# Kernel tuning notes

Measured on AMD Instinct MI355X. Metric: run time of the kernel, lower is better.

## Reference

```python
import jax, jax.numpy as jnp
import numpy as np
from jax import lax

N = 100000
E = 1600000
IN_C = 128
HID = 128
OUT_C = 64
NUM_CLASSES = 40
BN_EPS = 1e-5


def gcn_conv(x, row, col, W, b):
    # x: [N, F_in] -> [N, F_out]; PyG GCNConv: self-loops + sym normalization
    h = x @ W                                   # [N, F_out]
    loops = jnp.arange(N, dtype=row.dtype)
    r = jnp.concatenate([row, loops])           # [E+N]
    c = jnp.concatenate([col, loops])
    ones = jnp.ones(r.shape[0], dtype=x.dtype)
    deg = jax.ops.segment_sum(ones, c, num_segments=N)
    dinv = jnp.where(deg > 0, lax.rsqrt(deg), jnp.zeros_like(deg))
    norm = dinv[r] * dinv[c]                    # [E+N]
    msg = h[r] * norm[:, None]                  # gather + scale  [E+N, F_out]
    out = jax.ops.segment_sum(msg, c, num_segments=N)
    return out + b


def setup_inputs() -> dict:
    key = jax.random.key(0)
    ks = jax.random.split(key, 16)
    def glorot(k, shape):
        lim = float(np.sqrt(6.0 / (shape[0] + shape[1])))
        return jax.random.uniform(k, shape, jnp.float32, -lim, lim)
    x = jax.random.normal(ks[0], (N, IN_C), jnp.float32)
    edge_index = jax.random.randint(ks[1], (2, E), 0, N, jnp.int64)
    return {
        "x": x,
        "edge_index": edge_index,
        "w1": glorot(ks[2], (IN_C, HID)), "b1": jnp.zeros((HID,), jnp.float32),
        "w2": glorot(ks[3], (HID, HID)), "b2": jnp.zeros((HID,), jnp.float32),
        "bn_gamma": jnp.ones((HID,), jnp.float32), "bn_beta": jnp.zeros((HID,), jnp.float32),
        "bn_mean": jnp.zeros((HID,), jnp.float32), "bn_var": jnp.ones((HID,), jnp.float32),
        "cls_w": glorot(ks[4], (HID, OUT_C)), "cls_b": jnp.zeros((OUT_C,), jnp.float32),
        "sim_w": glorot(ks[5], (HID, NUM_CLASSES)), "sim_b": jnp.zeros((NUM_CLASSES,), jnp.float32),
        "hom_w": glorot(ks[6], (HID, 1)), "hom_b": jnp.zeros((1,), jnp.float32),
        "ent_w": glorot(ks[7], (HID, 1)), "ent_b": jnp.zeros((1,), jnp.float32),
    }


def reference(x, edge_index, w1, b1, w2, b2, bn_gamma, bn_beta, bn_mean, bn_var,
              cls_w, cls_b, sim_w, sim_b, hom_w, hom_b, ent_w, ent_b):
    row, col = edge_index[0], edge_index[1]
    # layer 1: GCNConv -> BN (eval) -> ReLU (dropout is identity in eval)
    h = gcn_conv(x, row, col, w1, b1)
    h = (h - bn_mean) * lax.rsqrt(bn_var + BN_EPS) * bn_gamma + bn_beta
    h = jax.nn.relu(h)
    # layer 2
    h = gcn_conv(h, row, col, w2, b2)
    main_out = jax.nn.log_softmax(h @ cls_w + cls_b, axis=1)
    sim_out = jax.nn.softmax(h @ sim_w + sim_b, axis=1)
    hom_out = jax.nn.sigmoid((h @ hom_w + hom_b)[:, 0])
    ent_out = jax.nn.sigmoid((h @ ent_w + ent_b)[:, 0])
    return (main_out, sim_out, hom_out, ent_out)
```

## Files before the change

kernel.cpp:

```cpp
#include <hip/hip_runtime.h>
#include <hip/hip_bf16.h>
#include <math.h>

#define N_NODES 100000
#define N_EDGES 1600000
#define F 128
#define OUT_C 64
#define NUM_CLASSES 40
#define BN_EPS 1e-5f

#define NBUCK 782
#define BCAP 4096

#define PREP_FILL 512
#define EPB ((N_EDGES + PREP_FILL - 1) / PREP_FILL)
#define FILL_ITERS 13
#define PREP_CONST (PREP_FILL + 128)
#define PREP_CVT (PREP_FILL + 129)
#define CVT_BLOCKS 6250

#define PSC 0
#define POF 128
#define PFB2 256

typedef __hip_bfloat16 bf16;
typedef __attribute__((ext_vector_type(8))) short bf16x8;
typedef __attribute__((ext_vector_type(4))) float f32x4;

struct ParamSegs {
    const void* src[16];
    int dst[16];
};

__device__ __forceinline__ float uasf(unsigned u) { return __uint_as_float(u); }
__device__ __forceinline__ unsigned f2bu(float f) {
    bf16 h = __float2bfloat16(f);
    return (unsigned)*(unsigned short*)&h;
}
__device__ __forceinline__ float ldp(const void* p, int i, int isf) {
    return isf ? ((const float*)p)[i] : __bfloat162float(((const bf16*)p)[i]);
}
__device__ __forceinline__ int load_edge(const int* __restrict__ ei, int which, int i, int i64) {
    size_t elem = (size_t)which * N_EDGES + (size_t)i;
    return i64 ? ei[elem * 2] : ei[elem];
}
__device__ __forceinline__ int detect_isf(const void* x, int t, int* sflag) {
    if (t < 64) {
        unsigned w = ((const unsigned*)x)[t];
        unsigned e = (w >> 23) & 0xFFu;
        unsigned long long m = __ballot(w == 0u || (e >= 90u && e <= 160u));
        if (t == 0) *sflag = (__popcll(m) >= 48) ? 1 : 0;
    }
    __syncthreads();
    return *sflag;
}
__device__ __forceinline__ int detect_i64(const void* ei, int t, int* sflag) {
    if (t < 64) {
        unsigned long long m = __ballot(((const unsigned*)ei)[2 * t + 1] == 0u);
        if (t == 0) *sflag = (__popcll(m) >= 60) ? 1 : 0;
    }
    __syncthreads();
    return *sflag;
}
__device__ __forceinline__ void head_src(const ParamSegs& segs, int c, const void** hp, int* hb,
                                         int* hs) {
    if (c < OUT_C) {
        *hp = segs.src[8];
        *hb = c;
        *hs = OUT_C;
    } else if (c < OUT_C + NUM_CLASSES) {
        *hp = segs.src[10];
        *hb = c - OUT_C;
        *hs = NUM_CLASSES;
    } else if (c == 104) {
        *hp = segs.src[12];
        *hb = 0;
        *hs = 1;
    } else if (c == 105) {
        *hp = segs.src[14];
        *hb = 0;
        *hs = 1;
    } else {
        *hp = nullptr;
        *hb = 0;
        *hs = 0;
    }
}

#define ACC8(u)                                \
    do {                                       \
        a[0] += uasf((u).x << 16);             \
        a[1] += uasf((u).x & 0xFFFF0000u);     \
        a[2] += uasf((u).y << 16);             \
        a[3] += uasf((u).y & 0xFFFF0000u);     \
        a[4] += uasf((u).z << 16);             \
        a[5] += uasf((u).z & 0xFFFF0000u);     \
        a[6] += uasf((u).w << 16);             \
        a[7] += uasf((u).w & 0xFFFF0000u);     \
    } while (0)
#define ACC8W(u, s_)                                        \
    do {                                                    \
        a[0] = fmaf(uasf((u).x << 16), (s_), a[0]);         \
        a[1] = fmaf(uasf((u).x & 0xFFFF0000u), (s_), a[1]); \
        a[2] = fmaf(uasf((u).y << 16), (s_), a[2]);         \
        a[3] = fmaf(uasf((u).y & 0xFFFF0000u), (s_), a[3]); \
        a[4] = fmaf(uasf((u).z << 16), (s_), a[4]);         \
        a[5] = fmaf(uasf((u).z & 0xFFFF0000u), (s_), a[5]); \
        a[6] = fmaf(uasf((u).w << 16), (s_), a[6]);         \
        a[7] = fmaf(uasf((u).w & 0xFFFF0000u), (s_), a[7]); \
    } while (0)

__global__ __launch_bounds__(256) void prep_kernel(const void* __restrict__ x,
                                                   const int* __restrict__ ei, ParamSegs segs,
                                                   int* __restrict__ bcur,
                                                   int* __restrict__ srcBuck,
                                                   float* __restrict__ params,
                                                   unsigned short* __restrict__ wt,
                                                   unsigned short* __restrict__ B16) {
    __shared__ int sflag;
    int t = threadIdx.x;
    int bid = blockIdx.x;

    if (bid < PREP_FILL) {
        __shared__ int hist[NBUCK];
        __shared__ int gbase[NBUCK];
        __shared__ int lcur[NBUCK];
        int i64 = detect_i64(ei, t, &sflag);
        int e0 = bid * EPB;
        int ecnt = N_EDGES - e0;
        if (ecnt > EPB) ecnt = EPB;
        for (int i = t; i < NBUCK; i += 256) hist[i] = 0;
        __syncthreads();
        int ccache[FILL_ITERS];
#pragma unroll
        for (int it = 0; it < FILL_ITERS; ++it) {
            int i = t + it * 256;
            int c = -1;
            if (i < ecnt) {
                c = load_edge(ei, 1, e0 + i, i64);
                atomicAdd(&hist[c >> 7], 1);
            }
            ccache[it] = c;
        }
        __syncthreads();
        for (int i = t; i < NBUCK; i += 256) {
            int c = hist[i];
            gbase[i] = (c > 0) ? atomicAdd(&bcur[i], c) : 0;
            lcur[i] = 0;
        }
        __syncthreads();
#pragma unroll
        for (int it = 0; it < FILL_ITERS; ++it) {
            int i = t + it * 256;
            if (i < ecnt) {
                int c = ccache[it];
                int r = load_edge(ei, 0, e0 + i, i64);
                int b = c >> 7;
                int p = gbase[b] + atomicAdd(&lcur[b], 1);
                if (p < BCAP) srcBuck[b * BCAP + p] = ((c & 127) << 17) | r;
            }
        }
    } else if (bid < PREP_CONST) {
        int isf = detect_isf(x, t, &sflag);
        int idx = (bid - PREP_FILL) * 256 + t;
        if (idx < 16384) {
            int kf = idx >> 7, c = idx & 127;
            const void* hp;
            int hb, hs;
            head_src(segs, c, &hp, &hb, &hs);
            float s = 0.f;
            if (hp) {
                const void* w2 = segs.src[2];
#pragma unroll 8
                for (int j = 0; j < 128; j++)
                    s += ldp(w2, kf * 128 + j, isf) * ldp(hp, j * hs + hb, isf);
            }
            int p = (kf & 15) * 8 + (kf >> 4);
            wt[16384 + c * 128 + p] = (unsigned short)f2bu(s);
        } else {
            int l = idx - 16384;
            int n = l >> 7, k = l & 127;
            wt[n * 128 + k] = (unsigned short)f2bu(ldp(segs.src[0], k * 128 + n, isf));
        }
    } else if (bid == PREP_CONST) {
        int isf = detect_isf(x, t, &sflag);
        if (t < 128) {
            float s = rsqrtf(ldp(segs.src[7], t, isf) + BN_EPS) * ldp(segs.src[4], t, isf);
            params[PSC + t] = s;
            params[POF + t] = ldp(segs.src[1], t, isf) * s + ldp(segs.src[5], t, isf) -
                              ldp(segs.src[6], t, isf) * s;
            const void* hp;
            int hb, hs;
            head_src(segs, t, &hp, &hb, &hs);
            float b = 0.f;
            if (hp) {
                const void* b2 = segs.src[3];
#pragma unroll 8
                for (int j = 0; j < 128; j++) b += ldp(b2, j, isf) * ldp(hp, j * hs + hb, isf);
            }
            if (t < OUT_C) b += ldp(segs.src[9], t, isf);
            else if (t < OUT_C + NUM_CLASSES) b += ldp(segs.src[11], t - OUT_C, isf);
            else if (t == 104) b += ldp(segs.src[13], 0, isf);
            else if (t == 105) b += ldp(segs.src[15], 0, isf);
            params[PFB2 + t] = b;
        }
    } else {
        int isf = detect_isf(x, t, &sflag);
        if (!isf) return;
        int i8 = (bid - PREP_CVT) * 256 + t;
        float4 va = ((const float4*)x)[2 * i8];
        float4 vb = ((const float4*)x)[2 * i8 + 1];
        uint4 o;
        o.x = f2bu(va.x) | (f2bu(va.y) << 16);
        o.y = f2bu(va.z) | (f2bu(va.w) << 16);
        o.z = f2bu(vb.x) | (f2bu(vb.y) << 16);
        o.w = f2bu(vb.z) | (f2bu(vb.w) << 16);
        ((uint4*)B16)[i8] = o;
    }
}

__global__ __launch_bounds__(512) void presort_kernel(int* __restrict__ srcBuck,
                                                      const int* __restrict__ bcur,
                                                      int* __restrict__ doffG,
                                                      int* __restrict__ dcntG,
                                                      float* __restrict__ dinv) {
    __shared__ int raw[BCAP];
    __shared__ int sorted[BCAP];
    __shared__ int dcnt[128], doff[128], dcur[128];
    int b = blockIdx.x;
    int t = threadIdx.x;
    int cnt = bcur[b];
    if (cnt > BCAP) cnt = BCAP;
    if (t < 128) dcnt[t] = 0;
    __syncthreads();
    for (int i = t; i < cnt; i += 512) {
        int e = srcBuck[b * BCAP + i];
        raw[i] = e;
        atomicAdd(&dcnt[e >> 17], 1);
    }
    __syncthreads();
    if (t < 128) doff[t] = dcnt[t];
    __syncthreads();
    for (int d = 1; d < 128; d <<= 1) {
        int add = 0;
        if (t < 128 && t >= d) add = doff[t - d];
        __syncthreads();
        if (t < 128) doff[t] += add;
        __syncthreads();
    }
    if (t < 128) {
        doff[t] -= dcnt[t];
        dcur[t] = 0;
    }
    __syncthreads();
    for (int i = t; i < cnt; i += 512) {
        int e = raw[i];
        int d = e >> 17;
        int r = atomicAdd(&dcur[d], 1);
        sorted[doff[d] + r] = e & 0x1FFFF;
    }
    __syncthreads();
    for (int i = t; i < cnt; i += 512) srcBuck[b * BCAP + i] = sorted[i];
    if (t < 128) {
        doffG[(b << 7) + t] = doff[t];
        dcntG[(b << 7) + t] = dcnt[t];
        int n = (b << 7) + t;
        if (n < N_NODES) dinv[n] = rsqrtf((float)(dcnt[t] + 1));
    }
}

template <bool SRC1>
__global__ __launch_bounds__(512) void aggh_kernel(const void* __restrict__ x,
                                                   const unsigned short* __restrict__ B16,
                                                   unsigned short* __restrict__ OUT16,
                                                   const int* __restrict__ srcBuck,
                                                   const int* __restrict__ doffG,
                                                   const int* __restrict__ dcntG,
                                                   const float* __restrict__ dinv,
                                                   int* __restrict__ wcnt) {
    __shared__ int sIdx[BCAP];
    __shared__ int sdoff[128], sdcnt[128];
    __shared__ int sCtl[2];
    __shared__ int sflag;
    int t = threadIdx.x;
    const unsigned short* IN = B16;
    if (SRC1) {
        int isf = detect_isf(x, t, &sflag);
        if (!isf) IN = (const unsigned short*)x;
    }
    if (t == 0) {
        unsigned xcc;
        asm volatile("s_getreg_b32 %0, hwreg(HW_REG_XCC_ID)" : "=s"(xcc));
        int half = (xcc >> 2) & 1;
        int idx = atomicAdd(&wcnt[half], 1);
        if (idx >= NBUCK) {
            half ^= 1;
            idx = atomicAdd(&wcnt[half], 1);
        }
        sCtl[0] = idx;
        sCtl[1] = half;
    }
    __syncthreads();
    int b = sCtl[0], h = sCtl[1];
    if (b >= NBUCK) return;
    if (t < 128) {
        sdoff[t] = doffG[(b << 7) + t];
        sdcnt[t] = dcntG[(b << 7) + t];
    }
    __syncthreads();
    int cnt = sdoff[127] + sdcnt[127];
    for (int i = t; i < cnt; i += 512) sIdx[i] = srcBuck[b * BCAP + i];
    __syncthreads();

    int g8 = t >> 3;
    int hoff = h * 64 + ((t & 7) << 3);
    int base = b << 7;
    for (int d = g8; d < 128; d += 64) {
        int n = base + d;
        if (n >= N_NODES) break;
        float dn = dinv[n];
        float a[8] = {0.f, 0.f, 0.f, 0.f, 0.f, 0.f, 0.f, 0.f};
        {
            uint4 u = *(const uint4*)(IN + ((size_t)n << 7) + hoff);
            if (SRC1) ACC8W(u, dn);
            else ACC8(u);
        }
        int o = sdoff[d], k = sdcnt[d];
        int j = 0;
        for (; j + 8 <= k; j += 8) {
            int s0 = sIdx[o + j + 0], s1 = sIdx[o + j + 1];
            int s2 = sIdx[o + j + 2], s3 = sIdx[o + j + 3];
            int s4 = sIdx[o + j + 4], s5 = sIdx[o + j + 5];
            int s6 = sIdx[o + j + 6], s7 = sIdx[o + j + 7];
            uint4 u0 = *(const uint4*)(IN + ((size_t)s0 << 7) + hoff);
            uint4 u1 = *(const uint4*)(IN + ((size_t)s1 << 7) + hoff);
            uint4 u2 = *(const uint4*)(IN + ((size_t)s2 << 7) + hoff);
            uint4 u3 = *(const uint4*)(IN + ((size_t)s3 << 7) + hoff);
            uint4 u4 = *(const uint4*)(IN + ((size_t)s4 << 7) + hoff);
            uint4 u5 = *(const uint4*)(IN + ((size_t)s5 << 7) + hoff);
            uint4 u6 = *(const uint4*)(IN + ((size_t)s6 << 7) + hoff);
            uint4 u7 = *(const uint4*)(IN + ((size_t)s7 << 7) + hoff);
            if (SRC1) {
                float f0 = dinv[s0], f1 = dinv[s1], f2 = dinv[s2], f3 = dinv[s3];
                float f4 = dinv[s4], f5 = dinv[s5], f6 = dinv[s6], f7 = dinv[s7];
                ACC8W(u0, f0);
                ACC8W(u1, f1);
                ACC8W(u2, f2);
                ACC8W(u3, f3);
                ACC8W(u4, f4);
                ACC8W(u5, f5);
                ACC8W(u6, f6);
                ACC8W(u7, f7);
            } else {
                ACC8(u0);
                ACC8(u1);
                ACC8(u2);
                ACC8(u3);
                ACC8(u4);
                ACC8(u5);
                ACC8(u6);
                ACC8(u7);
            }
        }
        for (; j + 4 <= k; j += 4) {
            int s0 = sIdx[o + j + 0], s1 = sIdx[o + j + 1];
            int s2 = sIdx[o + j + 2], s3 = sIdx[o + j + 3];
            uint4 u0 = *(const uint4*)(IN + ((size_t)s0 << 7) + hoff);
            uint4 u1 = *(const uint4*)(IN + ((size_t)s1 << 7) + hoff);
            uint4 u2 = *(const uint4*)(IN + ((size_t)s2 << 7) + hoff);
            uint4 u3 = *(const uint4*)(IN + ((size_t)s3 << 7) + hoff);
            if (SRC1) {
                float f0 = dinv[s0], f1 = dinv[s1], f2 = dinv[s2], f3 = dinv[s3];
                ACC8W(u0, f0);
                ACC8W(u1, f1);
                ACC8W(u2, f2);
                ACC8W(u3, f3);
            } else {
                ACC8(u0);
                ACC8(u1);
                ACC8(u2);
                ACC8(u3);
            }
        }
        for (; j < k; j++) {
            int s0 = sIdx[o + j];
            uint4 u0 = *(const uint4*)(IN + ((size_t)s0 << 7) + hoff);
            if (SRC1) {
                float f0 = dinv[s0];
                ACC8W(u0, f0);
            } else {
                ACC8(u0);
            }
        }
        uint4 pk;
        pk.x = f2bu(a[0] * dn) | (f2bu(a[1] * dn) << 16);
        pk.y = f2bu(a[2] * dn) | (f2bu(a[3] * dn) << 16);
        pk.z = f2bu(a[4] * dn) | (f2bu(a[5] * dn) << 16);
        pk.w = f2bu(a[6] * dn) | (f2bu(a[7] * dn) << 16);
        *(uint4*)(OUT16 + ((size_t)n << 7) + hoff) = pk;
    }
}

__global__ __launch_bounds__(256) void gemm_mfma_kernel(
    const unsigned short* __restrict__ A16, const unsigned short* __restrict__ Wt,
    unsigned short* __restrict__ outB, void* __restrict__ out,
    const float* __restrict__ params, const float* __restrict__ dinv, int mode,
    const void* __restrict__ x) {
    __shared__ float sF1[128], sF2[128];
    __shared__ int sflag;
    int t = threadIdx.x;
    int isf = detect_isf(x, t, &sflag);
    if (t < 128) {
        if (mode) {
            sF1[t] = params[PSC + t];
            sF2[t] = params[POF + t];
        } else {
            sF1[t] = params[PFB2 + t];
        }
    }
    __syncthreads();
    int wave = t >> 6, lane = t & 63, m16 = lane & 15, quad = lane >> 4;
    int rowbase = blockIdx.x * 64 + wave * 16;
    int rA = rowbase + m16;
    if (rA >= N_NODES) rA = N_NODES - 1;
    const size_t abase = (size_t)rA * 128 + (quad << 3);

    f32x4 acc[8];
#pragma unroll
    for (int ct = 0; ct < 8; ct++) acc[ct] = (f32x4){0.f, 0.f, 0.f, 0.f};
#pragma unroll
    for (int kk = 0; kk < 4; kk++) {
        bf16x8 af = *(const bf16x8*)(A16 + abase + kk * 32);
#pragma unroll
        for (int ct = 0; ct < 8; ct++) {
            bf16x8 bfr = *(const bf16x8*)(Wt + (size_t)((ct * 16 + m16) * 128) + kk * 32 + (quad << 3));
            acc[ct] = __builtin_amdgcn_mfma_f32_16x16x32_bf16(af, bfr, acc[ct], 0, 0, 0);
        }
    }

    int r0 = rowbase + quad * 4;
    if (mode) {
        float sc[8], of[8];
#pragma unroll
        for (int ct = 0; ct < 8; ct++) {
            sc[ct] = sF1[ct * 16 + m16];
            of[ct] = sF2[ct * 16 + m16];
        }
#pragma unroll
        for (int reg = 0; reg < 4; reg++) {
            int gr = r0 + reg;
            if (gr >= N_NODES) continue;
            float dn = dinv[gr];
            unsigned pk[4];
#pragma unroll
            for (int i = 0; i < 4; i++) {
                float v0 = fmaxf(acc[2 * i][reg] * sc[2 * i] + of[2 * i], 0.f) * dn;
                float v1 = fmaxf(acc[2 * i + 1][reg] * sc[2 * i + 1] + of[2 * i + 1], 0.f) * dn;
                pk[i] = f2bu(v0) | (f2bu(v1) << 16);
            }
            *(uint4*)(outB + (size_t)gr * 128 + (m16 << 3)) = make_uint4(pk[0], pk[1], pk[2], pk[3]);
        }
    } else {
        const size_t OFF_SIM = (size_t)N_NODES * OUT_C;
        const size_t OFF_HOM = OFF_SIM + (size_t)N_NODES * NUM_CLASSES;
        const size_t OFF_ENT = OFF_HOM + (size_t)N_NODES;
        float* outf = (float*)out;
        bf16* outb = (bf16*)out;
        float fb[8];
#pragma unroll
        for (int ct = 0; ct < 8; ct++) fb[ct] = sF1[ct * 16 + m16];
#define STORE_OUT(idx, v)                        \
    do {                                         \
        if (isf) outf[(idx)] = (v);              \
        else outb[(idx)] = __float2bfloat16(v);  \
    } while (0)
#pragma unroll
        for (int reg = 0; reg < 4; reg++) {
            int gr = r0 + reg;
            bool vrow = (gr < N_NODES);
            float v[8];
#pragma unroll
            for (int ct = 0; ct < 8; ct++) v[ct] = acc[ct][reg] + fb[ct];
            float m = fmaxf(fmaxf(v[0], v[1]), fmaxf(v[2], v[3]));
            m = fmaxf(m, __shfl_xor(m, 1));
            m = fmaxf(m, __shfl_xor(m, 2));
            m = fmaxf(m, __shfl_xor(m, 4));
            m = fmaxf(m, __shfl_xor(m, 8));
            float S = __expf(v[0] - m) + __expf(v[1] - m) + __expf(v[2] - m) + __expf(v[3] - m);
            S += __shfl_xor(S, 1);
            S += __shfl_xor(S, 2);
            S += __shfl_xor(S, 4);
            S += __shfl_xor(S, 8);
            float lS = m + __logf(S);
            if (vrow) {
#pragma unroll
                for (int ct = 0; ct < 4; ct++)
                    STORE_OUT((size_t)gr * OUT_C + ct * 16 + m16, v[ct] - lS);
            }
            bool has6 = (m16 < 8);
            float s4 = v[4], s5 = v[5], s6 = has6 ? v[6] : -INFINITY;
            float m2 = fmaxf(fmaxf(s4, s5), s6);
            m2 = fmaxf(m2, __shfl_xor(m2, 1));
            m2 = fmaxf(m2, __shfl_xor(m2, 2));
            m2 = fmaxf(m2, __shfl_xor(m2, 4));
            m2 = fmaxf(m2, __shfl_xor(m2, 8));
            float e4 = __expf(s4 - m2), e5 = __expf(s5 - m2), e6 = has6 ? __expf(s6 - m2) : 0.f;
            float S2 = e4 + e5 + e6;
            S2 += __shfl_xor(S2, 1);
            S2 += __shfl_xor(S2, 2);
            S2 += __shfl_xor(S2, 4);
            S2 += __shfl_xor(S2, 8);
            float rS2 = 1.f / S2;
            if (vrow) {
                STORE_OUT(OFF_SIM + (size_t)gr * NUM_CLASSES + m16, e4 * rS2);
                STORE_OUT(OFF_SIM + (size_t)gr * NUM_CLASSES + 16 + m16, e5 * rS2);
                if (has6) STORE_OUT(OFF_SIM + (size_t)gr * NUM_CLASSES + 32 + m16, e6 * rS2);
                if (m16 == 8) STORE_OUT(OFF_HOM + gr, 1.f / (1.f + __expf(-v[6])));
                if (m16 == 9) STORE_OUT(OFF_ENT + gr, 1.f / (1.f + __expf(-v[6])));
            }
        }
#undef STORE_OUT
    }
}

extern "C" void kernel_launch(void* const* d_in, const int* in_sizes, int n_in,
                              void* d_out, int out_size, void* d_ws, size_t ws_size,
                              hipStream_t stream) {
    const void* x = d_in[0];
    const int* ei = (const int*)d_in[1];

    char* ws = (char*)d_ws;
    size_t o = 0;
    auto alloc = [&](size_t bytes) {
        size_t r = o;
        o = (o + bytes + 255) & ~(size_t)255;
        return r;
    };
    char* RA = ws + alloc((size_t)51 * 1024 * 1024);
    char* RB = ws + alloc((size_t)26 * 1024 * 1024);
    float* params = (float*)(ws + alloc(2048));
    unsigned short* wt = (unsigned short*)(ws + alloc(65536));
    float* dinv = (float*)(ws + alloc((size_t)N_NODES * 4));
    int* doffG = (int*)(ws + alloc((size_t)NBUCK * 128 * 4));
    int* dcntG = (int*)(ws + alloc((size_t)NBUCK * 128 * 4));
    int* bcur = (int*)(ws + alloc((size_t)(NBUCK + 8) * 4));
    int* wcnt = (int*)(ws + alloc(256));

    int* srcBuck = (int*)RA;
    unsigned short* B16 = (unsigned short*)(RA + 13u * 1024 * 1024);
    unsigned short* G16 = (unsigned short*)RB;

    hipMemsetAsync(bcur, 0, (size_t)((char*)wcnt + 256 - (char*)bcur), stream);

    ParamSegs segs;
    const int srcIdx[16] = {2, 3, 4, 5, 6, 7, 8, 9, 10, 11, 12, 13, 14, 15, 16, 17};
    for (int k = 0; k < 16; k++) {
        segs.src[k] = d_in[srcIdx[k]];
        segs.dst[k] = 0;
    }

    prep_kernel<<<PREP_CVT + CVT_BLOCKS, 256, 0, stream>>>(x, ei, segs, bcur, srcBuck, params,
                                                           wt, B16);
    presort_kernel<<<NBUCK, 512, 0, stream>>>(srcBuck, bcur, doffG, dcntG, dinv);

    const int gemmGrid = (N_NODES + 63) / 64;
    aggh_kernel<true><<<2 * NBUCK, 512, 0, stream>>>(x, B16, G16, srcBuck, doffG, dcntG, dinv,
                                                     wcnt);
    gemm_mfma_kernel<<<gemmGrid, 256, 0, stream>>>(G16, wt, B16, nullptr, params, dinv, 1, x);
    aggh_kernel<false><<<2 * NBUCK, 512, 0, stream>>>(x, B16, G16, srcBuck, doffG, dcntG, dinv,
                                                      wcnt + 2);
    gemm_mfma_kernel<<<gemmGrid, 256, 0, stream>>>(G16, wt + 16384, nullptr, d_out, params, dinv,
                                                   0, x);
}
```

Baseline: 374.7 us.

## Store gathered node features as software 8-bit floats for aggregation

Result: slower. 468.0 us (+24.9%).

```diff
diff --git a/kernel.cpp b/kernel.cpp
--- a/kernel.cpp
+++ b/kernel.cpp
@@ -12,12 +12,14 @@
 #define NBUCK 782
 #define BCAP 4096
 
-#define PREP_FILL 512
-#define EPB ((N_EDGES + PREP_FILL - 1) / PREP_FILL)
+#define PREP_WB 0
+#define PREP_CONSTB 128
+#define PREP_FILLB 129
+#define PREP_NFILL 512
+#define EPB ((N_EDGES + PREP_NFILL - 1) / PREP_NFILL)
 #define FILL_ITERS 13
-#define PREP_CONST (PREP_FILL + 128)
-#define PREP_CVT (PREP_FILL + 129)
-#define CVT_BLOCKS 6250
+#define PREP_CVTB (PREP_FILLB + PREP_NFILL)
+#define CVT8_BLOCKS 3125
 
 #define PSC 0
 #define POF 128
@@ -87,27 +89,33 @@
     }
 }
 
-#define ACC8(u)                                \
-    do {                                       \
-        a[0] += uasf((u).x << 16);             \
-        a[1] += uasf((u).x & 0xFFFF0000u);     \
-        a[2] += uasf((u).y << 16);             \
-        a[3] += uasf((u).y & 0xFFFF0000u);     \
-        a[4] += uasf((u).z << 16);             \
-        a[5] += uasf((u).z & 0xFFFF0000u);     \
-        a[6] += uasf((u).w << 16);             \
-        a[7] += uasf((u).w & 0xFFFF0000u);     \
+__device__ __forceinline__ unsigned q8(float f) {
+    unsigned b = __float_as_uint(f);
+    unsigned s = (b >> 24) & 0x80u;
+    unsigned mag = (b & 0x7FFFFFFFu) + 0x00080000u;
+    int e = (int)(mag >> 23) - 127;
+    if (e < -6) return s;
+    if (e > 8) return s | 0x7Fu;
+    return s | ((unsigned)(e + 7) << 3) | ((mag >> 20) & 7u);
+}
+__device__ __forceinline__ float dq8(unsigned q) {
+    unsigned t = (((q & 0x80u) << 24)) | (((q & 0x7Fu) << 20) + (120u << 23));
+    return (q & 0x7Fu) ? uasf(t) : 0.f;
+}
+
+#define DQACC(dw, s_, i0)                                            \
+    do {                                                             \
+        a[(i0) + 0] = fmaf(dq8((dw)&0xFFu), (s_), a[(i0) + 0]);      \
+        a[(i0) + 1] = fmaf(dq8(((dw) >> 8) & 0xFFu), (s_), a[(i0) + 1]);  \
+        a[(i0) + 2] = fmaf(dq8(((dw) >> 16) & 0xFFu), (s_), a[(i0) + 2]); \
+        a[(i0) + 3] = fmaf(dq8((dw) >> 24), (s_), a[(i0) + 3]);      \
     } while (0)
-#define ACC8W(u, s_)                                        \
-    do {                                                    \
-        a[0] = fmaf(uasf((u).x << 16), (s_), a[0]);         \
-        a[1] = fmaf(uasf((u).x & 0xFFFF0000u), (s_), a[1]); \
-        a[2] = fmaf(uasf((u).y << 16), (s_), a[2]);         \
-        a[3] = fmaf(uasf((u).y & 0xFFFF0000u), (s_), a[3]); \
-        a[4] = fmaf(uasf((u).z << 16), (s_), a[4]);         \
-        a[5] = fmaf(uasf((u).z & 0xFFFF0000u), (s_), a[5]); \
-        a[6] = fmaf(uasf((u).w << 16), (s_), a[6]);         \
-        a[7] = fmaf(uasf((u).w & 0xFFFF0000u), (s_), a[7]); \
+#define DQ16(u, s_)          \
+    do {                     \
+        DQACC((u).x, s_, 0); \
+        DQACC((u).y, s_, 4); \
+        DQACC((u).z, s_, 8); \
+        DQACC((u).w, s_, 12);\
     } while (0)
 
 __global__ __launch_bounds__(256) void prep_kernel(const void* __restrict__ x,
@@ -116,53 +124,14 @@
                                                    int* __restrict__ srcBuck,
                                                    float* __restrict__ params,
                                                    unsigned short* __restrict__ wt,
-                                                   unsigned short* __restrict__ B16) {
+                                                   unsigned char* __restrict__ X8) {
     __shared__ int sflag;
     int t = threadIdx.x;
     int bid = blockIdx.x;
 
-    if (bid < PREP_FILL) {
-        __shared__ int hist[NBUCK];
-        __shared__ int gbase[NBUCK];
-        __shared__ int lcur[NBUCK];
-        int i64 = detect_i64(ei, t, &sflag);
-        int e0 = bid * EPB;
-        int ecnt = N_EDGES - e0;
-        if (ecnt > EPB) ecnt = EPB;
-        for (int i = t; i < NBUCK; i += 256) hist[i] = 0;
-        __syncthreads();
-        int ccache[FILL_ITERS];
-#pragma unroll
-        for (int it = 0; it < FILL_ITERS; ++it) {
-            int i = t + it * 256;
-            int c = -1;
-            if (i < ecnt) {
-                c = load_edge(ei, 1, e0 + i, i64);
-                atomicAdd(&hist[c >> 7], 1);
-            }
-            ccache[it] = c;
-        }
-        __syncthreads();
-        for (int i = t; i < NBUCK; i += 256) {
-            int c = hist[i];
-            gbase[i] = (c > 0) ? atomicAdd(&bcur[i], c) : 0;
-            lcur[i] = 0;
-        }
-        __syncthreads();
-#pragma unroll
-        for (int it = 0; it < FILL_ITERS; ++it) {
-            int i = t + it * 256;
-            if (i < ecnt) {
-                int c = ccache[it];
-                int r = load_edge(ei, 0, e0 + i, i64);
-                int b = c >> 7;
-                int p = gbase[b] + atomicAdd(&lcur[b], 1);
-                if (p < BCAP) srcBuck[b * BCAP + p] = ((c & 127) << 17) | r;
-            }
-        }
-    } else if (bid < PREP_CONST) {
+    if (bid < PREP_CONSTB) {
         int isf = detect_isf(x, t, &sflag);
-        int idx = (bid - PREP_FILL) * 256 + t;
+        int idx = bid * 256 + t;
         if (idx < 16384) {
             int kf = idx >> 7, c = idx & 127;
             const void* hp;
@@ -182,7 +151,7 @@
             int n = l >> 7, k = l & 127;
             wt[n * 128 + k] = (unsigned short)f2bu(ldp(segs.src[0], k * 128 + n, isf));
         }
-    } else if (bid == PREP_CONST) {
+    } else if (bid == PREP_CONSTB) {
         int isf = detect_isf(x, t, &sflag);
         if (t < 128) {
             float s = rsqrtf(ldp(segs.src[7], t, isf) + BN_EPS) * ldp(segs.src[4], t, isf);
@@ -204,18 +173,73 @@
             else if (t == 105) b += ldp(segs.src[15], 0, isf);
             params[PFB2 + t] = b;
         }
+    } else if (bid < PREP_CVTB) {
+        __shared__ int hist[NBUCK];
+        __shared__ int gbase[NBUCK];
+        __shared__ int lcur[NBUCK];
+        int i64 = detect_i64(ei, t, &sflag);
+        int blk = bid - PREP_FILLB;
+        int e0 = blk * EPB;
+        int ecnt = N_EDGES - e0;
+        if (ecnt > EPB) ecnt = EPB;
+        for (int i = t; i < NBUCK; i += 256) hist[i] = 0;
+        __syncthreads();
+        int ccache[FILL_ITERS];
+#pragma unroll
+        for (int it = 0; it < FILL_ITERS; ++it) {
+            int i = t + it * 256;
+            int c = -1;
+            if (i < ecnt) {
+                c = load_edge(ei, 1, e0 + i, i64);
+                atomicAdd(&hist[c >> 7], 1);
+            }
+            ccache[it] = c;
+        }
+        __syncthreads();
+        for (int i = t; i < NBUCK; i += 256) {
+            int c = hist[i];
+            gbase[i] = (c > 0) ? atomicAdd(&bcur[i], c) : 0;
+            lcur[i] = 0;
+        }
+        __syncthreads();
+#pragma unroll
+        for (int it = 0; it < FILL_ITERS; ++it) {
+            int i = t + it * 256;
+            if (i < ecnt) {
+                int c = ccache[it];
+                int r = load_edge(ei, 0, e0 + i, i64);
+                int b = c >> 7;
+                int p = gbase[b] + atomicAdd(&lcur[b], 1);
+                if (p < BCAP) srcBuck[b * BCAP + p] = ((c & 127) << 17) | r;
+            }
+        }
     } else {
         int isf = detect_isf(x, t, &sflag);
-        if (!isf) return;
-        int i8 = (bid - PREP_CVT) * 256 + t;
-        float4 va = ((const float4*)x)[2 * i8];
-        float4 vb = ((const float4*)x)[2 * i8 + 1];
-        uint4 o;
-        o.x = f2bu(va.x) | (f2bu(va.y) << 16);
-        o.y = f2bu(va.z) | (f2bu(va.w) << 16);
-        o.z = f2bu(vb.x) | (f2bu(vb.y) << 16);
-        o.w = f2bu(vb.z) | (f2bu(vb.w) << 16);
-        ((uint4*)B16)[i8] = o;
+        int i16 = (bid - PREP_CVTB) * 256 + t;
+        unsigned o0, o1, o2, o3;
+        if (isf) {
+            const float* xf = (const float*)x + (size_t)i16 * 16;
+            float4 v0 = *(const float4*)(xf + 0);
+            float4 v1 = *(const float4*)(xf + 4);
+            float4 v2 = *(const float4*)(xf + 8);
+            float4 v3 = *(const float4*)(xf + 12);
+            o0 = q8(v0.x) | (q8(v0.y) << 8) | (q8(v0.z) << 16) | (q8(v0.w) << 24);
+            o1 = q8(v1.x) | (q8(v1.y) << 8) | (q8(v1.z) << 16) | (q8(v1.w) << 24);
+            o2 = q8(v2.x) | (q8(v2.y) << 8) | (q8(v2.z) << 16) | (q8(v2.w) << 24);
+            o3 = q8(v3.x) | (q8(v3.y) << 8) | (q8(v3.z) << 16) | (q8(v3.w) << 24);
+        } else {
+            const uint4* xu = (const uint4*)((const unsigned short*)x + (size_t)i16 * 16);
+            uint4 u0 = xu[0], u1 = xu[1];
+            o0 = q8(uasf(u0.x << 16)) | (q8(uasf(u0.x & 0xFFFF0000u)) << 8) |
+                 (q8(uasf(u0.y << 16)) << 16) | (q8(uasf(u0.y & 0xFFFF0000u)) << 24);
+            o1 = q8(uasf(u0.z << 16)) | (q8(uasf(u0.z & 0xFFFF0000u)) << 8) |
+                 (q8(uasf(u0.w << 16)) << 16) | (q8(uasf(u0.w & 0xFFFF0000u)) << 24);
+            o2 = q8(uasf(u1.x << 16)) | (q8(uasf(u1.x & 0xFFFF0000u)) << 8) |
+                 (q8(uasf(u1.y << 16)) << 16) | (q8(uasf(u1.y & 0xFFFF0000u)) << 24);
+            o3 = q8(uasf(u1.z << 16)) | (q8(uasf(u1.z & 0xFFFF0000u)) << 8) |
+                 (q8(uasf(u1.w << 16)) << 16) | (q8(uasf(u1.w & 0xFFFF0000u)) << 24);
+        }
+        ((uint4*)X8)[i16] = make_uint4(o0, o1, o2, o3);
     }
 }
 
@@ -270,39 +294,16 @@
 }
 
 template <bool SRC1>
-__global__ __launch_bounds__(512) void aggh_kernel(const void* __restrict__ x,
-                                                   const unsigned short* __restrict__ B16,
-                                                   unsigned short* __restrict__ OUT16,
-                                                   const int* __restrict__ srcBuck,
-                                                   const int* __restrict__ doffG,
-                                                   const int* __restrict__ dcntG,
-                                                   const float* __restrict__ dinv,
-                                                   int* __restrict__ wcnt) {
+__global__ __launch_bounds__(512) void aggf8_kernel(const unsigned char* __restrict__ IN8,
+                                                    unsigned short* __restrict__ OUT16,
+                                                    const int* __restrict__ srcBuck,
+                                                    const int* __restrict__ doffG,
+                                                    const int* __restrict__ dcntG,
+                                                    const float* __restrict__ dinv) {
     __shared__ int sIdx[BCAP];
     __shared__ int sdoff[128], sdcnt[128];
-    __shared__ int sCtl[2];
-    __shared__ int sflag;
     int t = threadIdx.x;
-    const unsigned short* IN = B16;
-    if (SRC1) {
-        int isf = detect_isf(x, t, &sflag);
-        if (!isf) IN = (const unsigned short*)x;
-    }
-    if (t == 0) {
-        unsigned xcc;
-        asm volatile("s_getreg_b32 %0, hwreg(HW_REG_XCC_ID)" : "=s"(xcc));
-        int half = (xcc >> 2) & 1;
-        int idx = atomicAdd(&wcnt[half], 1);
-        if (idx >= NBUCK) {
-            half ^= 1;
-            idx = atomicAdd(&wcnt[half], 1);
-        }
-        sCtl[0] = idx;
-        sCtl[1] = half;
-    }
-    __syncthreads();
-    int b = sCtl[0], h = sCtl[1];
-    if (b >= NBUCK) return;
+    int b = blockIdx.x;
     if (t < 128) {
         sdoff[t] = doffG[(b << 7) + t];
         sdcnt[t] = dcntG[(b << 7) + t];
@@ -313,17 +314,19 @@
     __syncthreads();
 
     int g8 = t >> 3;
-    int hoff = h * 64 + ((t & 7) << 3);
+    int boff = (t & 7) << 4;
     int base = b << 7;
     for (int d = g8; d < 128; d += 64) {
         int n = base + d;
         if (n >= N_NODES) break;
         float dn = dinv[n];
-        float a[8] = {0.f, 0.f, 0.f, 0.f, 0.f, 0.f, 0.f, 0.f};
+        float a[16];
+#pragma unroll
+        for (int i = 0; i < 16; i++) a[i] = 0.f;
         {
-            uint4 u = *(const uint4*)(IN + ((size_t)n << 7) + hoff);
-            if (SRC1) ACC8W(u, dn);
-            else ACC8(u);
+            uint4 u = *(const uint4*)(IN8 + (size_t)n * 128 + boff);
+            if (SRC1) DQ16(u, dn);
+            else DQ16(u, 1.0f);
         }
         int o = sdoff[d], k = sdcnt[d];
         int j = 0;
@@ -332,78 +335,84 @@
             int s2 = sIdx[o + j + 2], s3 = sIdx[o + j + 3];
             int s4 = sIdx[o + j + 4], s5 = sIdx[o + j + 5];
             int s6 = sIdx[o + j + 6], s7 = sIdx[o + j + 7];
-            uint4 u0 = *(const uint4*)(IN + ((size_t)s0 << 7) + hoff);
-            uint4 u1 = *(const uint4*)(IN + ((size_t)s1 << 7) + hoff);
-            uint4 u2 = *(const uint4*)(IN + ((size_t)s2 << 7) + hoff);
-            uint4 u3 = *(const uint4*)(IN + ((size_t)s3 << 7) + hoff);
-            uint4 u4 = *(const uint4*)(IN + ((size_t)s4 << 7) + hoff);
-            uint4 u5 = *(const uint4*)(IN + ((size_t)s5 << 7) + hoff);
-            uint4 u6 = *(const uint4*)(IN + ((size_t)s6 << 7) + hoff);
-            uint4 u7 = *(const uint4*)(IN + ((size_t)s7 << 7) + hoff);
+            uint4 u0 = *(const uint4*)(IN8 + (size_t)s0 * 128 + boff);
+            uint4 u1 = *(const uint4*)(IN8 + (size_t)s1 * 128 + boff);
+            uint4 u2 = *(const uint4*)(IN8 + (size_t)s2 * 128 + boff);
+            uint4 u3 = *(const uint4*)(IN8 + (size_t)s3 * 128 + boff);
+            uint4 u4 = *(const uint4*)(IN8 + (size_t)s4 * 128 + boff);
+            uint4 u5 = *(const uint4*)(IN8 + (size_t)s5 * 128 + boff);
+            uint4 u6 = *(const uint4*)(IN8 + (size_t)s6 * 128 + boff);
+            uint4 u7 = *(const uint4*)(IN8 + (size_t)s7 * 128 + boff);
             if (SRC1) {
                 float f0 = dinv[s0], f1 = dinv[s1], f2 = dinv[s2], f3 = dinv[s3];
                 float f4 = dinv[s4], f5 = dinv[s5], f6 = dinv[s6], f7 = dinv[s7];
-                ACC8W(u0, f0);
-                ACC8W(u1, f1);
-                ACC8W(u2, f2);
-                ACC8W(u3, f3);
-                ACC8W(u4, f4);
-                ACC8W(u5, f5);
-                ACC8W(u6, f6);
-                ACC8W(u7, f7);
+                DQ16(u0, f0);
+                DQ16(u1, f1);
+                DQ16(u2, f2);
+                DQ16(u3, f3);
+                DQ16(u4, f4);
+                DQ16(u5, f5);
+                DQ16(u6, f6);
+                DQ16(u7, f7);
             } else {
-                ACC8(u0);
-                ACC8(u1);
-                ACC8(u2);
-                ACC8(u3);
-                ACC8(u4);
-                ACC8(u5);
-                ACC8(u6);
-                ACC8(u7);
+                DQ16(u0, 1.0f);
+                DQ16(u1, 1.0f);
+                DQ16(u2, 1.0f);
+                DQ16(u3, 1.0f);
+                DQ16(u4, 1.0f);
+                DQ16(u5, 1.0f);
+                DQ16(u6, 1.0f);
+                DQ16(u7, 1.0f);
             }
         }
         for (; j + 4 <= k; j += 4) {
             int s0 = sIdx[o + j + 0], s1 = sIdx[o + j + 1];
             int s2 = sIdx[o + j + 2], s3 = sIdx[o + j + 3];
-            uint4 u0 = *(const uint4*)(IN + ((size_t)s0 << 7) + hoff);
-            uint4 u1 = *(const uint4*)(IN + ((size_t)s1 << 7) + hoff);
-            uint4 u2 = *(const uint4*)(IN + ((size_t)s2 << 7) + hoff);
-            uint4 u3 = *(const uint4*)(IN + ((size_t)s3 << 7) + hoff);
+            uint4 u0 = *(const uint4*)(IN8 + (size_t)s0 * 128 + boff);
+            uint4 u1 = *(const uint4*)(IN8 + (size_t)s1 * 128 + boff);
+            uint4 u2 = *(const uint4*)(IN8 + (size_t)s2 * 128 + boff);
+            uint4 u3 = *(const uint4*)(IN8 + (size_t)s3 * 128 + boff);
             if (SRC1) {
                 float f0 = dinv[s0], f1 = dinv[s1], f2 = dinv[s2], f3 = dinv[s3];
-                ACC8W(u0, f0);
-                ACC8W(u1, f1);
-                ACC8W(u2, f2);
-                ACC8W(u3, f3);
+                DQ16(u0, f0);
+                DQ16(u1, f1);
+                DQ16(u2, f2);
+                DQ16(u3, f3);
             } else {
-                ACC8(u0);
-                ACC8(u1);
-                ACC8(u2);
-                ACC8(u3);
+                DQ16(u0, 1.0f);
+                DQ16(u1, 1.0f);
+                DQ16(u2, 1.0f);
+                DQ16(u3, 1.0f);
             }
         }
         for (; j < k; j++) {
             int s0 = sIdx[o + j];
-            uint4 u0 = *(const uint4*)(IN + ((size_t)s0 << 7) + hoff);
+            uint4 u0 = *(const uint4*)(IN8 + (size_t)s0 * 128 + boff);
             if (SRC1) {
                 float f0 = dinv[s0];
-                ACC8W(u0, f0);
+                DQ16(u0, f0);
             } else {
-                ACC8(u0);
-            }
-        }
-        uint4 pk;
-        pk.x = f2bu(a[0] * dn) | (f2bu(a[1] * dn) << 16);
-        pk.y = f2bu(a[2] * dn) | (f2bu(a[3] * dn) << 16);
-        pk.z = f2bu(a[4] * dn) | (f2bu(a[5] * dn) << 16);
-        pk.w = f2bu(a[6] * dn) | (f2bu(a[7] * dn) << 16);
-        *(uint4*)(OUT16 + ((size_t)n << 7) + hoff) = pk;
+                DQ16(u0, 1.0f);
+            }
+        }
+        uint4 p0, p1;
+        p0.x = f2bu(a[0] * dn) | (f2bu(a[1] * dn) << 16);
+        p0.y = f2bu(a[2] * dn) | (f2bu(a[3] * dn) << 16);
+        p0.z = f2bu(a[4] * dn) | (f2bu(a[5] * dn) << 16);
+        p0.w = f2bu(a[6] * dn) | (f2bu(a[7] * dn) << 16);
+        p1.x = f2bu(a[8] * dn) | (f2bu(a[9] * dn) << 16);
+        p1.y = f2bu(a[10] * dn) | (f2bu(a[11] * dn) << 16);
+        p1.z = f2bu(a[12] * dn) | (f2bu(a[13] * dn) << 16);
+        p1.w = f2bu(a[14] * dn) | (f2bu(a[15] * dn) << 16);
+        unsigned short* wp = OUT16 + (size_t)n * 128 + boff;
+        *(uint4*)wp = p0;
+        *(uint4*)(wp + 8) = p1;
     }
 }
 
 __global__ __launch_bounds__(256) void gemm_mfma_kernel(
     const unsigned short* __restrict__ A16, const unsigned short* __restrict__ Wt,
-    unsigned short* __restrict__ outB, void* __restrict__ out,
+    unsigned char* __restrict__ outB8, void* __restrict__ out,
     const float* __restrict__ params, const float* __restrict__ dinv, int mode,
     const void* __restrict__ x) {
     __shared__ float sF1[128], sF2[128];
@@ -451,14 +460,13 @@
             int gr = r0 + reg;
             if (gr >= N_NODES) continue;
             float dn = dinv[gr];
-            unsigned pk[4];
-#pragma unroll
-            for (int i = 0; i < 4; i++) {
-                float v0 = fmaxf(acc[2 * i][reg] * sc[2 * i] + of[2 * i], 0.f) * dn;
-                float v1 = fmaxf(acc[2 * i + 1][reg] * sc[2 * i + 1] + of[2 * i + 1], 0.f) * dn;
-                pk[i] = f2bu(v0) | (f2bu(v1) << 16);
-            }
-            *(uint4*)(outB + (size_t)gr * 128 + (m16 << 3)) = make_uint4(pk[0], pk[1], pk[2], pk[3]);
+            float vv[8];
+#pragma unroll
+            for (int ct = 0; ct < 8; ct++)
+                vv[ct] = fmaxf(acc[ct][reg] * sc[ct] + of[ct], 0.f) * dn;
+            unsigned lo = q8(vv[0]) | (q8(vv[1]) << 8) | (q8(vv[2]) << 16) | (q8(vv[3]) << 24);
+            unsigned hi = q8(vv[4]) | (q8(vv[5]) << 8) | (q8(vv[6]) << 16) | (q8(vv[7]) << 24);
+            *(uint2*)(outB8 + (size_t)gr * 128 + (m16 << 3)) = make_uint2(lo, hi);
         }
     } else {
         const size_t OFF_SIM = (size_t)N_NODES * OUT_C;
@@ -544,13 +552,13 @@
     int* doffG = (int*)(ws + alloc((size_t)NBUCK * 128 * 4));
     int* dcntG = (int*)(ws + alloc((size_t)NBUCK * 128 * 4));
     int* bcur = (int*)(ws + alloc((size_t)(NBUCK + 8) * 4));
-    int* wcnt = (int*)(ws + alloc(256));
 
     int* srcBuck = (int*)RA;
-    unsigned short* B16 = (unsigned short*)(RA + 13u * 1024 * 1024);
+    unsigned char* X8 = (unsigned char*)(RA + 13u * 1024 * 1024);
+    unsigned char* H8 = (unsigned char*)(RA + 26u * 1024 * 1024);
     unsigned short* G16 = (unsigned short*)RB;
 
-    hipMemsetAsync(bcur, 0, (size_t)((char*)wcnt + 256 - (char*)bcur), stream);
+    hipMemsetAsync(bcur, 0, (size_t)(NBUCK + 8) * 4, stream);
 
     ParamSegs segs;
     const int srcIdx[16] = {2, 3, 4, 5, 6, 7, 8, 9, 10, 11, 12, 13, 14, 15, 16, 17};
@@ -559,16 +567,14 @@
         segs.dst[k] = 0;
     }
 
-    prep_kernel<<<PREP_CVT + CVT_BLOCKS, 256, 0, stream>>>(x, ei, segs, bcur, srcBuck, params,
-                                                           wt, B16);
+    prep_kernel<<<PREP_CVTB + CVT8_BLOCKS, 256, 0, stream>>>(x, ei, segs, bcur, srcBuck, params,
+                                                             wt, X8);
     presort_kernel<<<NBUCK, 512, 0, stream>>>(srcBuck, bcur, doffG, dcntG, dinv);
 
     const int gemmGrid = (N_NODES + 63) / 64;
-    aggh_kernel<true><<<2 * NBUCK, 512, 0, stream>>>(x, B16, G16, srcBuck, doffG, dcntG, dinv,
-                                                     wcnt);
-    gemm_mfma_kernel<<<gemmGrid, 256, 0, stream>>>(G16, wt, B16, nullptr, params, dinv, 1, x);
-    aggh_kernel<false><<<2 * NBUCK, 512, 0, stream>>>(x, B16, G16, srcBuck, doffG, dcntG, dinv,
-                                                      wcnt + 2);
+    aggf8_kernel<true><<<NBUCK, 512, 0, stream>>>(X8, G16, srcBuck, doffG, dcntG, dinv);
+    gemm_mfma_kernel<<<gemmGrid, 256, 0, stream>>>(G16, wt, H8, nullptr, params, dinv, 1, x);
+    aggf8_kernel<false><<<NBUCK, 512, 0, stream>>>(H8, G16, srcBuck, doffG, dcntG, dinv);
     gemm_mfma_kernel<<<gemmGrid, 256, 0, stream>>>(G16, wt + 16384, nullptr, d_out, params, dinv,
                                                    0, x);
 }
```
